# Kernel tuning notes

Measured on AMD Instinct MI355X. Metric: run time of the kernel, lower is better.

Reference implementation:

```python
import jax, jax.numpy as jnp
import numpy as np

N = 100000
E = 1250000
D = 64
K = 3
A_COEF = 1.0
B_COEF = 1.0
L_DOM = -1.0
R_DOM = 1.0


def setup_inputs() -> dict:
    key = jax.random.key(0)
    k1, k2, k3, k4, k5 = jax.random.split(key, 5)
    x = jax.random.normal(k1, (N, D), dtype=jnp.float32)
    edge_index = jax.random.randint(k2, (2, E), 0, N, dtype=jnp.int64)
    edge_weight = jax.random.uniform(k3, (E,), dtype=jnp.float32)
    alpha_params = jnp.ones((K + 1,), dtype=jnp.float32)
    lin_w = jax.random.normal(k4, ((K + 1) * D, D), dtype=jnp.float32) / np.sqrt((K + 1) * D)
    lin_b = jnp.zeros((D,), dtype=jnp.float32)
    return {"x": x, "edge_index": edge_index, "edge_weight": edge_weight,
            "alpha_params": alpha_params, "lin_w": lin_w, "lin_b": lin_b}


def reference(x, edge_index, edge_weight, alpha_params, lin_w, lin_b):
    row, col = edge_index[0], edge_index[1]
    # gcn normalization: deg from source nodes, deg<0.5 -> +1
    deg = jax.ops.segment_sum(jnp.ones((E,), x.dtype), row, num_segments=N)
    deg = jnp.where(deg < 0.5, deg + 1.0, deg)
    dis = deg ** -0.5
    val = dis[row] * edge_weight * dis[col]  # [E]

    def spmm(h):  # adj @ h : out[row] += val * h[col]
        return jax.ops.segment_sum(val[:, None] * h[col], row, num_segments=N)

    alphas = jnp.tanh(alpha_params)  # basealpha = 1.0
    a, b, l, r = A_COEF, B_COEF, L_DOM, R_DOM
    xs = [x]
    for L in range(1, K + 1):
        Ax = spmm(xs[-1])
        if L == 1:
            coef1 = (a - b) / 2 - (a + b + 2) / 2 * ((l + r) / (r - l))
            coef2 = (a + b + 2) / (r - l)
            nxt = alphas[0] * (coef1 * xs[-1] + coef2 * Ax)
        else:
            coef_l = 2 * L * (L + a + b) * (2 * L - 2 + a + b)
            coef_lm1_1 = (2 * L + a + b - 1) * (2 * L + a + b) * (2 * L + a + b - 2)
            coef_lm1_2 = (2 * L + a + b - 1) * (a ** 2 - b ** 2)
            coef_lm2 = 2 * (L - 1 + a) * (L - 1 + b) * (2 * L + a + b)
            tmp1 = alphas[L - 1] * (coef_lm1_1 / coef_l)
            tmp2 = alphas[L - 1] * (coef_lm1_2 / coef_l)
            tmp3 = alphas[L - 1] * alphas[L - 2] * (coef_lm2 / coef_l)
            tmp1_2 = tmp1 * (2.0 / (r - l))
            tmp2_2 = tmp1 * ((r + l) / (r - l)) + tmp2
            nxt = tmp1_2 * Ax - tmp2_2 * xs[-1] - tmp3 * xs[-2]
        xs.append(nxt)
    x_cat = jnp.concatenate(xs, axis=1)  # [N, (K+1)*D]
    return x_cat @ lin_w + lin_b
```

## Files before the change

### kernel.cpp

```cpp
#include <hip/hip_runtime.h>
#include <hip/hip_bf16.h>
#include <math.h>

#define NN 100000
#define EE 1250000
#define DD 64

typedef __attribute__((ext_vector_type(8))) short short8;
typedef __attribute__((ext_vector_type(8))) unsigned short u16x8;
typedef __attribute__((ext_vector_type(4))) float f32x4;

__device__ __forceinline__ unsigned short f2b(float f) {
    unsigned u = __float_as_uint(f);
    u += 0x7fffu + ((u >> 16) & 1u);
    return (unsigned short)(u >> 16);
}
__device__ __forceinline__ float b2f(unsigned short h) {
    return __uint_as_float(((unsigned)h) << 16);
}

__global__ __launch_bounds__(256) void scan_a(const int* __restrict__ degi,
                                              int* __restrict__ rowStart,
                                              int* __restrict__ bs, int N) {
    __shared__ int s[256];
    int tid = threadIdx.x;
    int i = blockIdx.x * 256 + tid;
    int v = (i < N) ? degi[i] : 0;
    s[tid] = v;
    __syncthreads();
    for (int off = 1; off < 256; off <<= 1) {
        int t = (tid >= off) ? s[tid - off] : 0;
        __syncthreads();
        s[tid] += t;
        __syncthreads();
    }
    if (i < N) rowStart[i] = s[tid] - v;
    if (tid == 255) bs[blockIdx.x] = s[255];
}

__global__ __launch_bounds__(512) void scan_b(int* __restrict__ bs, int nb) {
    __shared__ int s[512];
    int tid = threadIdx.x;
    int v = (tid < nb) ? bs[tid] : 0;
    s[tid] = v;
    __syncthreads();
    for (int off = 1; off < 512; off <<= 1) {
        int t = (tid >= off) ? s[tid - off] : 0;
        __syncthreads();
        s[tid] += t;
        __syncthreads();
    }
    if (tid < nb) bs[tid] = s[tid] - v;
}

__global__ __launch_bounds__(256) void scan_c(int* __restrict__ rowStart,
                                              const int* __restrict__ bs,
                                              int N, int E) {
    int i = blockIdx.x * 256 + threadIdx.x;
    if (i < N) rowStart[i] += bs[blockIdx.x];
    if (i == 0) rowStart[N] = E;
}

__global__ __launch_bounds__(256) void dis_kernel(const int* __restrict__ degi,
                                                  float* __restrict__ dis, int N) {
    int i = blockIdx.x * 256 + threadIdx.x;
    if (i >= N) return;
    int d = degi[i];
    float df = (d == 0) ? 1.0f : (float)d;
    dis[i] = 1.0f / sqrtf(df);
}

#define NSL 125
#define SLR 800
#define NSEG 16
#define SEGCAP 768
#define CPAD 16
#define VSCL (1.0f / 32768.0f)
__global__ __launch_bounds__(256) void binA(const int* __restrict__ row,
                                            const int* __restrict__ col,
                                            const float* __restrict__ w,
                                            uint2* __restrict__ sbuf,
                                            int* __restrict__ segCnt, int E4) {
    __shared__ int cnt[NSL];
    __shared__ int base[NSL];
    int tid = threadIdx.x;
    if (tid < NSL) cnt[tid] = 0;
    __syncthreads();
    int g = blockIdx.x & (NSEG - 1);
    int i4 = blockIdx.x * 256 + tid;
    bool act = (i4 < E4);
    int4 r4, c4;
    float4 w4;
    int sl[4], loc[4], rk[4];
    unsigned evp[4];
    if (act) {
        r4 = ((const int4*)row)[i4];
        c4 = ((const int4*)col)[i4];
        w4 = ((const float4*)w)[i4];
        int rr[4] = {r4.x, r4.y, r4.z, r4.w};
        int cc[4] = {c4.x, c4.y, c4.z, c4.w};
        float ww[4] = {w4.x, w4.y, w4.z, w4.w};
        #pragma unroll
        for (int k = 0; k < 4; ++k) {
            int r = rr[k], c = cc[k];
            int wq = (int)(ww[k] * 32768.0f + 0.5f);
            wq = (wq > 32767) ? 32767 : wq;
            evp[k] = ((unsigned)c << 15) | (unsigned)wq;
            rk[k] = r;
            sl[k] = r / SLR;
            loc[k] = atomicAdd(&cnt[sl[k]], 1);
        }
    }
    __syncthreads();
    if (tid < NSL) {
        int c = cnt[tid];
        if (c) base[tid] = atomicAdd(&segCnt[(tid * NSEG + g) * CPAD], c);
    }
    __syncthreads();
    if (act) {
        #pragma unroll
        for (int k = 0; k < 4; ++k) {
            int p = base[sl[k]] + loc[k];
            if (p < SEGCAP)
                sbuf[(size_t)(sl[k] * NSEG + g) * SEGCAP + p] =
                    make_uint2(evp[k], (unsigned)rk[k]);
        }
    }
}

__global__ __launch_bounds__(512) void deg_slice(const uint2* __restrict__ sbuf,
                                                 const int* __restrict__ segCnt,
                                                 int* __restrict__ degi) {
    __shared__ int dcnt[SLR];
    __shared__ int scnt[NSEG];
    int tid = threadIdx.x;
    int s = blockIdx.x;
    int r0 = s * SLR;
    for (int i = tid; i < SLR; i += 512) dcnt[i] = 0;
    if (tid < NSEG) {
        int c = segCnt[(s * NSEG + tid) * CPAD];
        scnt[tid] = (c > SEGCAP) ? SEGCAP : c;
    }
    __syncthreads();
    for (int slot = tid * 4; slot < NSEG * SEGCAP; slot += 2048) {
        int g = slot / SEGCAP;
        int off = slot - g * SEGCAP;
        int cg = scnt[g];
        if (off >= cg) continue;
        const uint2* seg = sbuf + (size_t)(s * NSEG + g) * SEGCAP;
        uint4 a = *(const uint4*)(seg + off);
        uint4 b = *(const uint4*)(seg + off + 2);
        atomicAdd(&dcnt[(int)a.y - r0], 1);
        if (off + 1 < cg) atomicAdd(&dcnt[(int)a.w - r0], 1);
        if (off + 2 < cg) atomicAdd(&dcnt[(int)b.y - r0], 1);
        if (off + 3 < cg) atomicAdd(&dcnt[(int)b.w - r0], 1);
    }
    __syncthreads();
    for (int i = tid; i < SLR; i += 512) {
        int gr = r0 + i;
        if (gr < NN) degi[gr] = dcnt[i];
    }
}

__global__ __launch_bounds__(512) void binB(const uint2* __restrict__ sbuf,
                                            const int* __restrict__ segCnt,
                                            const int* __restrict__ rowStart,
                                            const float* __restrict__ dis,
                                            unsigned* __restrict__ ev) {
    __shared__ int curs[SLR];
    __shared__ int rs[SLR];
    __shared__ float dsl[SLR];
    __shared__ int scnt[NSEG];
    int tid = threadIdx.x;
    int s = blockIdx.x;
    int r0 = s * SLR;
    for (int i = tid; i < SLR; i += 512) {
        curs[i] = 0;
        int gr = r0 + i;
        rs[i] = (gr < NN) ? rowStart[gr] : 0;
        dsl[i] = (gr < NN) ? dis[gr] : 1.0f;
    }
    if (tid < NSEG) {
        int c = segCnt[(s * NSEG + tid) * CPAD];
        scnt[tid] = (c > SEGCAP) ? SEGCAP : c;
    }
    __syncthreads();
    for (int slot = tid * 4; slot < NSEG * SEGCAP; slot += 2048) {
        int g = slot / SEGCAP;
        int off = slot - g * SEGCAP;
        int cg = scnt[g];
        if (off >= cg) continue;
        const uint2* seg = sbuf + (size_t)(s * NSEG + g) * SEGCAP;
        uint4 a = *(const uint4*)(seg + off);
        uint4 b = *(const uint4*)(seg + off + 2);
        unsigned pk[4] = {a.x, a.z, b.x, b.z};
        unsigned rr[4] = {a.y, a.w, b.y, b.w};
        int nv = cg - off;
        nv = (nv > 4) ? 4 : nv;
        #pragma unroll 4
        for (int k = 0; k < 4; ++k) {
            if (k >= nv) break;
            int rl = (int)rr[k] - r0;
            int c = (int)(pk[k] >> 15);
            float wv = (float)(pk[k] & 0x7fffu) * VSCL;
            float v = dsl[rl] * wv * dis[c];
            int vq = (int)(v * 32768.0f + 0.5f);
            vq = (vq > 32767) ? 32767 : vq;
            ev[rs[rl] + atomicAdd(&curs[rl], 1)] = ((unsigned)c << 15) | (unsigned)vq;
        }
    }
}

__global__ void coef_kernel(const float* __restrict__ ap, float* __restrict__ coef) {
    if (threadIdx.x != 0 || blockIdx.x != 0) return;
    const float a = 1.0f, b = 1.0f, l = -1.0f, r = 1.0f;
    float als[3];
    als[0] = tanhf(ap[0]);
    als[1] = tanhf(ap[1]);
    als[2] = tanhf(ap[2]);
    float coef1 = (a - b) * 0.5f - (a + b + 2.0f) * 0.5f * ((l + r) / (r - l));
    float coef2 = (a + b + 2.0f) / (r - l);
    coef[0] = als[0] * coef1;
    coef[1] = als[0] * coef2;
    for (int L = 2; L <= 3; ++L) {
        float Lf = (float)L;
        float coef_l     = 2.0f * Lf * (Lf + a + b) * (2.0f * Lf - 2.0f + a + b);
        float coef_lm1_1 = (2.0f * Lf + a + b - 1.0f) * (2.0f * Lf + a + b) * (2.0f * Lf + a + b - 2.0f);
        float coef_lm1_2 = (2.0f * Lf + a + b - 1.0f) * (a * a - b * b);
        float coef_lm2   = 2.0f * (Lf - 1.0f + a) * (Lf - 1.0f + b) * (2.0f * Lf + a + b);
        float tmp1   = als[L - 1] * (coef_lm1_1 / coef_l);
        float tmp2   = als[L - 1] * (coef_lm1_2 / coef_l);
        float tmp3   = als[L - 1] * als[L - 2] * (coef_lm2 / coef_l);
        float tmp1_2 = tmp1 * (2.0f / (r - l));
        float tmp2_2 = tmp1 * ((r + l) / (r - l)) + tmp2;
        int base = 2 + (L - 2) * 3;
        coef[base + 0] = tmp1_2;
        coef[base + 1] = tmp2_2;
        coef[base + 2] = tmp3;
    }
}

__global__ __launch_bounds__(256) void tobf16(const float4* __restrict__ in,
                                              ushort4* __restrict__ outb, int n4) {
    int i = blockIdx.x * 256 + threadIdx.x;
    if (i >= n4) return;
    float4 v = in[i];
    ushort4 o;
    o.x = f2b(v.x); o.y = f2b(v.y); o.z = f2b(v.z); o.w = f2b(v.w);
    outb[i] = o;
}

__global__ __launch_bounds__(256) void wt_kernel(const float* __restrict__ W,
                                                 unsigned short* __restrict__ Wt) {
    int idx = blockIdx.x * 256 + threadIdx.x;
    int n = idx >> 8, k = idx & 255;
    Wt[idx] = f2b(W[k * 64 + n]);
}

__device__ __forceinline__ void fma8(float* a, unsigned u, u16x8 h) {
    float v = (float)(u & 0x7fffu) * VSCL;
    #pragma unroll
    for (int c = 0; c < 8; ++c) a[c] += v * b2f(h[c]);
}

template <int MODE>
__global__ __launch_bounds__(256) void spmm_fused(const int* __restrict__ rowStart,
                                                  const unsigned* __restrict__ ev,
                                                  const unsigned short* __restrict__ hb,
                                                  const unsigned short* __restrict__ xm1,
                                                  const unsigned short* __restrict__ xm2,
                                                  unsigned short* __restrict__ outb,
                                                  const float* __restrict__ coef,
                                                  int cbase, int N) {
    int t = blockIdx.x * 256 + threadIdx.x;
    int r = t >> 3;
    if (r >= N) return;
    int q = t & 7;
    int s0 = rowStart[r];
    int s1 = rowStart[r + 1];
    float a[8];
    #pragma unroll
    for (int c = 0; c < 8; ++c) a[c] = 0.f;
    int j = s0;
    for (; j + 3 < s1; j += 4) {
        unsigned u0 = ev[j];
        unsigned u1 = ev[j + 1];
        unsigned u2 = ev[j + 2];
        unsigned u3 = ev[j + 3];
        u16x8 h0 = *(const u16x8*)&hb[(size_t)(u0 >> 15) * 64 + q * 8];
        u16x8 h1 = *(const u16x8*)&hb[(size_t)(u1 >> 15) * 64 + q * 8];
        u16x8 h2 = *(const u16x8*)&hb[(size_t)(u2 >> 15) * 64 + q * 8];
        u16x8 h3 = *(const u16x8*)&hb[(size_t)(u3 >> 15) * 64 + q * 8];
        fma8(a, u0, h0);
        fma8(a, u1, h1);
        fma8(a, u2, h2);
        fma8(a, u3, h3);
    }
    for (; j < s1; ++j) {
        unsigned u0 = ev[j];
        u16x8 h0 = *(const u16x8*)&hb[(size_t)(u0 >> 15) * 64 + q * 8];
        fma8(a, u0, h0);
    }
    size_t oi = (size_t)r * 64 + q * 8;
    float o[8];
    if (MODE == 0) {
        float c0 = coef[cbase], c1 = coef[cbase + 1];
        u16x8 m1 = *(const u16x8*)&xm1[oi];
        #pragma unroll
        for (int c = 0; c < 8; ++c) o[c] = c0 * b2f(m1[c]) + c1 * a[c];
    } else {
        float c0 = coef[cbase], c1 = coef[cbase + 1], c2 = coef[cbase + 2];
        u16x8 m1 = *(const u16x8*)&xm1[oi];
        u16x8 m2 = *(const u16x8*)&xm2[oi];
        #pragma unroll
        for (int c = 0; c < 8; ++c)
            o[c] = c0 * a[c] - c1 * b2f(m1[c]) - c2 * b2f(m2[c]);
    }
    u16x8 ob;
    #pragma unroll
    for (int c = 0; c < 8; ++c) ob[c] = f2b(o[c]);
    *(u16x8*)&outb[oi] = ob;
}

__global__ __launch_bounds__(256, 4) void final_gemm_mfma(
        const ushort4* __restrict__ x0,
        const ushort4* __restrict__ x1,
        const ushort4* __restrict__ x2,
        const ushort4* __restrict__ x3,
        const unsigned short* __restrict__ Wt,
        const float* __restrict__ bias,
        float* __restrict__ out) {
    const int tid = threadIdx.x;
    const int lane = tid & 63;
    const int w = tid >> 6;
    const int m = lane & 15;
    const int quad = lane >> 4;
    const int n0 = (int)blockIdx.x * 128;

    int gr0 = n0 + 16 * w + m;
    int gr1 = gr0 + 64;
    size_t ar0 = (size_t)((gr0 < NN) ? gr0 : 0) * 16;
    size_t ar1 = (size_t)((gr1 < NN) ? gr1 : 0) * 16;

    f32x4 acc0[4], acc1[4];
    #pragma unroll
    for (int nt = 0; nt < 4; ++nt) {
        acc0[nt] = (f32x4){0.f, 0.f, 0.f, 0.f};
        acc1[nt] = (f32x4){0.f, 0.f, 0.f, 0.f};
    }

    #pragma unroll
    for (int ks = 0; ks < 8; ++ks) {
        const ushort4* p = (ks < 2) ? x0 : (ks < 4) ? x1 : (ks < 6) ? x2 : x3;
        size_t ko = (size_t)((ks & 1) * 8 + quad * 2);
        short8 af0 = *(const short8*)&p[ar0 + ko];
        short8 af1 = *(const short8*)&p[ar1 + ko];
        #pragma unroll
        for (int nt = 0; nt < 4; ++nt) {
            short8 bf = *(const short8*)&Wt[(nt * 16 + m) * 256 + ks * 32 + quad * 8];
            acc0[nt] = __builtin_amdgcn_mfma_f32_16x16x32_bf16(af0, bf, acc0[nt], 0, 0, 0);
            acc1[nt] = __builtin_amdgcn_mfma_f32_16x16x32_bf16(af1, bf, acc1[nt], 0, 0, 0);
        }
    }

    #pragma unroll
    for (int nt = 0; nt < 4; ++nt) {
        float bv = bias[nt * 16 + m];
        #pragma unroll
        for (int rg = 0; rg < 4; ++rg) {
            int node0 = n0 + 16 * w + quad * 4 + rg;
            int node1 = node0 + 64;
            if (node0 < NN) out[(size_t)node0 * 64 + nt * 16 + m] = acc0[nt][rg] + bv;
            if (node1 < NN) out[(size_t)node1 * 64 + nt * 16 + m] = acc1[nt][rg] + bv;
        }
    }
}

extern "C" void kernel_launch(void* const* d_in, const int* in_sizes, int n_in,
                              void* d_out, int out_size, void* d_ws, size_t ws_size,
                              hipStream_t stream) {
    const float* x  = (const float*)d_in[0];
    const int*   ei = (const int*)d_in[1];
    const float* ew = (const float*)d_in[2];
    const float* ap = (const float*)d_in[3];
    const float* lw = (const float*)d_in[4];
    const float* lb = (const float*)d_in[5];
    float* out = (float*)d_out;

    const int N = NN, E = EE;
    const int ND = N * DD;

    const int* row = ei;
    const int* col = ei + E;

    char* ws = (char*)d_ws;
    ushort4* xb = (ushort4*)ws;
    ushort4* Ab = (ushort4*)(ws + (size_t)ND * 2);
    ushort4* Bb = (ushort4*)(ws + (size_t)ND * 4);
    ushort4* Cb = (ushort4*)(ws + (size_t)ND * 6);
    uint2*   sbuf   = (uint2*)(ws + (size_t)ND * 4);
    int*     segCnt = (int*)(ws + (size_t)ND * 6);
    unsigned* ev = (unsigned*)(ws + (size_t)ND * 8);
    char* sm    = ws + (size_t)ND * 8 + (size_t)E * 4;
    float* coef     = (float*)sm;
    float* dis      = (float*)(sm + 256);
    int*   degi     = (int*)(sm + 256 + (size_t)N * 4);
    int*   rowStart = (int*)(sm + 256 + (size_t)N * 8);
    int*   bs       = (int*)(sm + 256 + (size_t)N * 12 + 64);
    unsigned short* Wt = (unsigned short*)(sm + 256 + (size_t)N * 12 + 64 + 4096);

    const int gridN  = (N + 255) / 256;
    const int gridSp = (N * 8) / 256;
    const int gridCv = (ND / 4) / 256;
    const int gridG  = (N + 127) / 128;
    const int E4     = E / 4;
    const int gridA  = (E4 + 255) / 256;

    hipMemsetAsync(segCnt, 0, (size_t)NSL * NSEG * CPAD * 4, stream);
    coef_kernel<<<1, 64, 0, stream>>>(ap, coef);
    wt_kernel<<<64, 256, 0, stream>>>(lw, Wt);
    binA<<<gridA, 256, 0, stream>>>(row, col, ew, sbuf, segCnt, E4);
    deg_slice<<<NSL, 512, 0, stream>>>(sbuf, segCnt, degi);
    scan_a<<<gridN, 256, 0, stream>>>(degi, rowStart, bs, N);
    scan_b<<<1, 512, 0, stream>>>(bs, gridN);
    scan_c<<<gridN, 256, 0, stream>>>(rowStart, bs, N, E);
    dis_kernel<<<gridN, 256, 0, stream>>>(degi, dis, N);
    binB<<<NSL, 512, 0, stream>>>(sbuf, segCnt, rowStart, dis, ev);

    tobf16<<<gridCv, 256, 0, stream>>>((const float4*)x, xb, ND / 4);

    spmm_fused<0><<<gridSp, 256, 0, stream>>>(rowStart, ev,
                                              (const unsigned short*)xb,
                                              (const unsigned short*)xb,
                                              (const unsigned short*)xb,
                                              (unsigned short*)Ab, coef, 0, N);
    spmm_fused<1><<<gridSp, 256, 0, stream>>>(rowStart, ev,
                                              (const unsigned short*)Ab,
                                              (const unsigned short*)Ab,
                                              (const unsigned short*)xb,
                                              (unsigned short*)Bb, coef, 2, N);
    spmm_fused<1><<<gridSp, 256, 0, stream>>>(rowStart, ev,
                                              (const unsigned short*)Bb,
                                              (const unsigned short*)Bb,
                                              (const unsigned short*)Ab,
                                              (unsigned short*)Cb, coef, 5, N);

    final_gemm_mfma<<<gridG, 256, 0, stream>>>(xb, Ab, Bb, Cb, Wt, lb, out);
}
```

Measured before the change: 251.9 us.

## Bucket CSR entries by column range within rows and unroll SpMM gather by eight

binB now makes an extra counting pass that histograms each row's edges into 13 column buckets (column >> 13), prefix-sums them from the row start, and scatters entries so that each row's neighbours are roughly ordered by column range. The aim is better locality in the gathered feature rows across warps during SpMM. The SpMM inner loop also gets an 8-way unrolled gather to put more loads in flight per thread. In exchange, binB reads the segment buffer twice, uses more shared memory, and the wider unroll raises register pressure.

```diff
diff --git a/kernel.cpp b/kernel.cpp
--- a/kernel.cpp
+++ b/kernel.cpp
@@ -75,6 +75,7 @@
 #define NSEG 16
 #define SEGCAP 768
 #define CPAD 16
+#define NCB 13
 #define VSCL (1.0f / 32768.0f)
 __global__ __launch_bounds__(256) void binA(const int* __restrict__ row,
                                             const int* __restrict__ col,
@@ -167,7 +168,7 @@
                                             const int* __restrict__ rowStart,
                                             const float* __restrict__ dis,
                                             unsigned* __restrict__ ev) {
-    __shared__ int curs[SLR];
+    __shared__ int cnt2[SLR][NCB];
     __shared__ int rs[SLR];
     __shared__ float dsl[SLR];
     __shared__ int scnt[NSEG];
@@ -175,14 +176,44 @@
     int s = blockIdx.x;
     int r0 = s * SLR;
     for (int i = tid; i < SLR; i += 512) {
-        curs[i] = 0;
         int gr = r0 + i;
         rs[i] = (gr < NN) ? rowStart[gr] : 0;
         dsl[i] = (gr < NN) ? dis[gr] : 1.0f;
+        #pragma unroll
+        for (int b = 0; b < NCB; ++b) cnt2[i][b] = 0;
     }
     if (tid < NSEG) {
         int c = segCnt[(s * NSEG + tid) * CPAD];
         scnt[tid] = (c > SEGCAP) ? SEGCAP : c;
+    }
+    __syncthreads();
+    for (int slot = tid * 4; slot < NSEG * SEGCAP; slot += 2048) {
+        int g = slot / SEGCAP;
+        int off = slot - g * SEGCAP;
+        int cg = scnt[g];
+        if (off >= cg) continue;
+        const uint2* seg = sbuf + (size_t)(s * NSEG + g) * SEGCAP;
+        uint4 a = *(const uint4*)(seg + off);
+        uint4 b = *(const uint4*)(seg + off + 2);
+        unsigned pk[4] = {a.x, a.z, b.x, b.z};
+        unsigned rr[4] = {a.y, a.w, b.y, b.w};
+        int nv = cg - off;
+        nv = (nv > 4) ? 4 : nv;
+        #pragma unroll 4
+        for (int k = 0; k < 4; ++k) {
+            if (k >= nv) break;
+            atomicAdd(&cnt2[(int)rr[k] - r0][(pk[k] >> 15) >> 13], 1);
+        }
+    }
+    __syncthreads();
+    for (int i = tid; i < SLR; i += 512) {
+        int run = rs[i];
+        #pragma unroll
+        for (int b = 0; b < NCB; ++b) {
+            int t = cnt2[i][b];
+            cnt2[i][b] = run;
+            run += t;
+        }
     }
     __syncthreads();
     for (int slot = tid * 4; slot < NSEG * SEGCAP; slot += 2048) {
@@ -206,7 +237,8 @@
             float v = dsl[rl] * wv * dis[c];
             int vq = (int)(v * 32768.0f + 0.5f);
             vq = (vq > 32767) ? 32767 : vq;
-            ev[rs[rl] + atomicAdd(&curs[rl], 1)] = ((unsigned)c << 15) | (unsigned)vq;
+            int pos = atomicAdd(&cnt2[rl][c >> 13], 1);
+            ev[pos] = ((unsigned)c << 15) | (unsigned)vq;
         }
     }
 }
@@ -282,6 +314,17 @@
     #pragma unroll
     for (int c = 0; c < 8; ++c) a[c] = 0.f;
     int j = s0;
+    for (; j + 7 < s1; j += 8) {
+        unsigned u[8];
+        u16x8 h[8];
+        #pragma unroll
+        for (int k = 0; k < 8; ++k) u[k] = ev[j + k];
+        #pragma unroll
+        for (int k = 0; k < 8; ++k)
+            h[k] = *(const u16x8*)&hb[(size_t)(u[k] >> 15) * 64 + q * 8];
+        #pragma unroll
+        for (int k = 0; k < 8; ++k) fma8(a, u[k], h[k]);
+    }
     for (; j + 3 < s1; j += 4) {
         unsigned u0 = ev[j];
         unsigned u1 = ev[j + 1];
```

Result: slower. 258.2 us (+2.5%).

## Split bf16 feature matrices into two 32-column planes and run SpMM per plane

Applied to the files above, without the earlier changes.

Each bf16 feature matrix is stored as two planes of 32 columns, and every SpMM hop runs as two launches, one per plane, with 4 threads per row instead of 8. Each plane is 6.4 MB instead of 12.8 MB, so the random gathers of h[col] can hit in cache more often. The cost is that the edge list and row pointers are read twice per hop and there are more kernel launches. The inner loop also gains an 8-way unrolled batch of gathers to keep more loads in flight, and the final GEMM indexes the planar layout.

```diff
diff --git a/kernel.cpp b/kernel.cpp
--- a/kernel.cpp
+++ b/kernel.cpp
@@ -247,7 +247,9 @@
     float4 v = in[i];
     ushort4 o;
     o.x = f2b(v.x); o.y = f2b(v.y); o.z = f2b(v.z); o.w = f2b(v.w);
-    outb[i] = o;
+    int n = i >> 4, d4 = i & 15;
+    int plane = d4 >> 3, po = d4 & 7;
+    outb[(size_t)plane * NN * 8 + (size_t)n * 8 + po] = o;
 }
 
 __global__ __launch_bounds__(256) void wt_kernel(const float* __restrict__ W,
@@ -273,24 +275,35 @@
                                                   const float* __restrict__ coef,
                                                   int cbase, int N) {
     int t = blockIdx.x * 256 + threadIdx.x;
-    int r = t >> 3;
+    int r = t >> 2;
     if (r >= N) return;
-    int q = t & 7;
+    int q = t & 3;
     int s0 = rowStart[r];
     int s1 = rowStart[r + 1];
     float a[8];
     #pragma unroll
     for (int c = 0; c < 8; ++c) a[c] = 0.f;
     int j = s0;
+    for (; j + 7 < s1; j += 8) {
+        unsigned u[8];
+        u16x8 h[8];
+        #pragma unroll
+        for (int k = 0; k < 8; ++k) u[k] = ev[j + k];
+        #pragma unroll
+        for (int k = 0; k < 8; ++k)
+            h[k] = *(const u16x8*)&hb[(size_t)(u[k] >> 15) * 32 + q * 8];
+        #pragma unroll
+        for (int k = 0; k < 8; ++k) fma8(a, u[k], h[k]);
+    }
     for (; j + 3 < s1; j += 4) {
         unsigned u0 = ev[j];
         unsigned u1 = ev[j + 1];
         unsigned u2 = ev[j + 2];
         unsigned u3 = ev[j + 3];
-        u16x8 h0 = *(const u16x8*)&hb[(size_t)(u0 >> 15) * 64 + q * 8];
-        u16x8 h1 = *(const u16x8*)&hb[(size_t)(u1 >> 15) * 64 + q * 8];
-        u16x8 h2 = *(const u16x8*)&hb[(size_t)(u2 >> 15) * 64 + q * 8];
-        u16x8 h3 = *(const u16x8*)&hb[(size_t)(u3 >> 15) * 64 + q * 8];
+        u16x8 h0 = *(const u16x8*)&hb[(size_t)(u0 >> 15) * 32 + q * 8];
+        u16x8 h1 = *(const u16x8*)&hb[(size_t)(u1 >> 15) * 32 + q * 8];
+        u16x8 h2 = *(const u16x8*)&hb[(size_t)(u2 >> 15) * 32 + q * 8];
+        u16x8 h3 = *(const u16x8*)&hb[(size_t)(u3 >> 15) * 32 + q * 8];
         fma8(a, u0, h0);
         fma8(a, u1, h1);
         fma8(a, u2, h2);
@@ -298,10 +311,10 @@
     }
     for (; j < s1; ++j) {
         unsigned u0 = ev[j];
-        u16x8 h0 = *(const u16x8*)&hb[(size_t)(u0 >> 15) * 64 + q * 8];
+        u16x8 h0 = *(const u16x8*)&hb[(size_t)(u0 >> 15) * 32 + q * 8];
         fma8(a, u0, h0);
     }
-    size_t oi = (size_t)r * 64 + q * 8;
+    size_t oi = (size_t)r * 32 + q * 8;
     float o[8];
     if (MODE == 0) {
         float c0 = coef[cbase], c1 = coef[cbase + 1];
@@ -323,10 +336,10 @@
 }
 
 __global__ __launch_bounds__(256, 4) void final_gemm_mfma(
-        const ushort4* __restrict__ x0,
-        const ushort4* __restrict__ x1,
-        const ushort4* __restrict__ x2,
-        const ushort4* __restrict__ x3,
+        const unsigned short* __restrict__ x0,
+        const unsigned short* __restrict__ x1,
+        const unsigned short* __restrict__ x2,
+        const unsigned short* __restrict__ x3,
         const unsigned short* __restrict__ Wt,
         const float* __restrict__ bias,
         float* __restrict__ out) {
@@ -339,8 +352,8 @@
 
     int gr0 = n0 + 16 * w + m;
     int gr1 = gr0 + 64;
-    size_t ar0 = (size_t)((gr0 < NN) ? gr0 : 0) * 16;
-    size_t ar1 = (size_t)((gr1 < NN) ? gr1 : 0) * 16;
+    size_t r0s = (size_t)((gr0 < NN) ? gr0 : 0) * 32;
+    size_t r1s = (size_t)((gr1 < NN) ? gr1 : 0) * 32;
 
     f32x4 acc0[4], acc1[4];
     #pragma unroll
@@ -351,10 +364,10 @@
 
     #pragma unroll
     for (int ks = 0; ks < 8; ++ks) {
-        const ushort4* p = (ks < 2) ? x0 : (ks < 4) ? x1 : (ks < 6) ? x2 : x3;
-        size_t ko = (size_t)((ks & 1) * 8 + quad * 2);
-        short8 af0 = *(const short8*)&p[ar0 + ko];
-        short8 af1 = *(const short8*)&p[ar1 + ko];
+        const unsigned short* p = (ks < 2) ? x0 : (ks < 4) ? x1 : (ks < 6) ? x2 : x3;
+        size_t pb = (size_t)(ks & 1) * NN * 32 + (size_t)quad * 8;
+        short8 af0 = *(const short8*)&p[pb + r0s];
+        short8 af1 = *(const short8*)&p[pb + r1s];
         #pragma unroll
         for (int nt = 0; nt < 4; ++nt) {
             short8 bf = *(const short8*)&Wt[(nt * 16 + m) * 256 + ks * 32 + quad * 8];
@@ -394,10 +407,10 @@
     const int* col = ei + E;
 
     char* ws = (char*)d_ws;
-    ushort4* xb = (ushort4*)ws;
-    ushort4* Ab = (ushort4*)(ws + (size_t)ND * 2);
-    ushort4* Bb = (ushort4*)(ws + (size_t)ND * 4);
-    ushort4* Cb = (ushort4*)(ws + (size_t)ND * 6);
+    unsigned short* xb = (unsigned short*)ws;
+    unsigned short* Ab = (unsigned short*)(ws + (size_t)ND * 2);
+    unsigned short* Bb = (unsigned short*)(ws + (size_t)ND * 4);
+    unsigned short* Cb = (unsigned short*)(ws + (size_t)ND * 6);
     uint2*   sbuf   = (uint2*)(ws + (size_t)ND * 4);
     int*     segCnt = (int*)(ws + (size_t)ND * 6);
     unsigned* ev = (unsigned*)(ws + (size_t)ND * 8);
@@ -410,11 +423,12 @@
     unsigned short* Wt = (unsigned short*)(sm + 256 + (size_t)N * 12 + 64 + 4096);
 
     const int gridN  = (N + 255) / 256;
-    const int gridSp = (N * 8) / 256;
+    const int gridSp = (N * 4 + 255) / 256;
     const int gridCv = (ND / 4) / 256;
     const int gridG  = (N + 127) / 128;
     const int E4     = E / 4;
     const int gridA  = (E4 + 255) / 256;
+    const size_t PL  = (size_t)NN * 32;
 
     hipMemsetAsync(segCnt, 0, (size_t)NSL * NSEG * CPAD * 4, stream);
     coef_kernel<<<1, 64, 0, stream>>>(ap, coef);
@@ -427,23 +441,20 @@
     dis_kernel<<<gridN, 256, 0, stream>>>(degi, dis, N);
     binB<<<NSL, 512, 0, stream>>>(sbuf, segCnt, rowStart, dis, ev);
 
-    tobf16<<<gridCv, 256, 0, stream>>>((const float4*)x, xb, ND / 4);
-
-    spmm_fused<0><<<gridSp, 256, 0, stream>>>(rowStart, ev,
-                                              (const unsigned short*)xb,
-                                              (const unsigned short*)xb,
-                                              (const unsigned short*)xb,
-                                              (unsigned short*)Ab, coef, 0, N);
-    spmm_fused<1><<<gridSp, 256, 0, stream>>>(rowStart, ev,
-                                              (const unsigned short*)Ab,
-                                              (const unsigned short*)Ab,
-                                              (const unsigned short*)xb,
-                                              (unsigned short*)Bb, coef, 2, N);
-    spmm_fused<1><<<gridSp, 256, 0, stream>>>(rowStart, ev,
-                                              (const unsigned short*)Bb,
-                                              (const unsigned short*)Bb,
-                                              (const unsigned short*)Ab,
-                                              (unsigned short*)Cb, coef, 5, N);
+    tobf16<<<gridCv, 256, 0, stream>>>((const float4*)x, (ushort4*)xb, ND / 4);
+
+    spmm_fused<0><<<gridSp, 256, 0, stream>>>(rowStart, ev, xb, xb, xb,
+                                              Ab, coef, 0, N);
+    spmm_fused<0><<<gridSp, 256, 0, stream>>>(rowStart, ev, xb + PL, xb + PL,
+                                              xb + PL, Ab + PL, coef, 0, N);
+    spmm_fused<1><<<gridSp, 256, 0, stream>>>(rowStart, ev, Ab, Ab, xb,
+                                              Bb, coef, 2, N);
+    spmm_fused<1><<<gridSp, 256, 0, stream>>>(rowStart, ev, Ab + PL, Ab + PL,
+                                              xb + PL, Bb + PL, coef, 2, N);
+    spmm_fused<1><<<gridSp, 256, 0, stream>>>(rowStart, ev, Bb, Bb, Ab,
+                                              Cb, coef, 5, N);
+    spmm_fused<1><<<gridSp, 256, 0, stream>>>(rowStart, ev, Bb + PL, Bb + PL,
+                                              Ab + PL, Cb + PL, coef, 5, N);
 
     final_gemm_mfma<<<gridG, 256, 0, stream>>>(xb, Ab, Bb, Cb, Wt, lb, out);
 }
```

New measurement: 288.3 us. 14.4% more time.
